# Performance work log

Measured on AMD Instinct MI355X. Metric: run time of the kernel, lower is better.

Reference implementation:

```python
import jax, jax.numpy as jnp
import numpy as np

DN = ('NCDHW', 'OIDHW', 'NCDHW')

def conv3d(x, w, b, stride=1, padding=1, lhs_dilation=1):
    pad = [(padding, padding)] * 3 if isinstance(padding, int) else padding
    y = jax.lax.conv_general_dilated(
        x, w, window_strides=(stride,) * 3, padding=pad,
        lhs_dilation=(lhs_dilation,) * 3, dimension_numbers=DN)
    return y + b[None, :, None, None, None]

def bool_to_multichannel(x):
    # (B,1,D,H,W) bool -> (B,8,D/4,H/4,W/4) float; each 4x4x4 patch bit-packed to 8 bytes
    B = x.shape[0]; D = x.shape[2]; d = D // 4
    p = x.reshape(B, d, 4, d, 4, d, 4)
    p = p.transpose(0, 1, 3, 5, 2, 4, 6).reshape(B, d, d, d, 8, 8)
    pw2 = (2.0 ** jnp.arange(8)).astype(jnp.float32)
    mc = jnp.sum(p.astype(jnp.float32) * pw2, axis=-1)  # (B,d,d,d,8)
    return mc.transpose(0, 4, 1, 2, 3) / 255.0

def setup_inputs():
    key = jax.random.key(0)
    ks = jax.random.split(key, 26)
    B, RES = 4, 256
    CH, E, ZC, K = 32, 16, 128, 8192
    L = 16  # latent resolution (mc res 64 / 2^(len(ch_mult)-1))
    # block-sparse boolean voxels so a good fraction of latent patches is all-zero
    coarse = jax.random.uniform(ks[0], (B, 1, 16, 16, 16)) < 0.6
    coarse = jnp.repeat(jnp.repeat(jnp.repeat(coarse, 16, 2), 16, 3), 16, 4)
    dense = jax.random.uniform(ks[1], (B, 1, RES, RES, RES)) < 0.3
    x = coarse & dense
    p = lambda k, shape, s=0.05: (jax.random.normal(k, shape) * s).astype(jnp.float32)
    return {
        'x': x,
        'enc_in_w': p(ks[2], (CH, 8, 3, 3, 3)), 'enc_in_b': p(ks[3], (CH,)),
        'enc_d1_w': p(ks[4], (2 * CH, CH, 3, 3, 3)), 'enc_d1_b': p(ks[5], (2 * CH,)),
        'enc_d2_w': p(ks[6], (4 * CH, 2 * CH, 3, 3, 3)), 'enc_d2_b': p(ks[7], (4 * CH,)),
        'enc_out_w': p(ks[8], (ZC, 4 * CH, 3, 3, 3)), 'enc_out_b': p(ks[9], (ZC,)),
        'quant_w': p(ks[10], (E, ZC, 1, 1, 1)), 'quant_b': p(ks[11], (E,)),
        'codebook': p(ks[12], (K, E), 0.5),
        'replacement_token': p(ks[13], (1, E), 0.02),
        'pos_embedding': p(ks[14], (1, E, L, L, L), 1.0),
        'post_quant_w': p(ks[15], (ZC, E, 1, 1, 1)), 'post_quant_b': p(ks[16], (ZC,)),
        'dec_in_w': p(ks[17], (ZC, ZC, 3, 3, 3)), 'dec_in_b': p(ks[18], (ZC,)),
        'dec_u1_w': p(ks[19], (2 * CH, ZC, 3, 3, 3)), 'dec_u1_b': p(ks[20], (2 * CH,)),
        'dec_u2_w': p(ks[21], (CH, 2 * CH, 3, 3, 3)), 'dec_u2_b': p(ks[22], (CH,)),
        'dec_out_w': p(ks[23], (8, CH, 3, 3, 3)), 'dec_out_b': p(ks[24], (8,)),
    }

def reference(x, enc_in_w, enc_in_b, enc_d1_w, enc_d1_b, enc_d2_w, enc_d2_b,
              enc_out_w, enc_out_b, quant_w, quant_b, codebook, replacement_token,
              pos_embedding, post_quant_w, post_quant_b, dec_in_w, dec_in_b,
              dec_u1_w, dec_u1_b, dec_u2_w, dec_u2_b, dec_out_w, dec_out_b):
    silu = jax.nn.silu
    mc = bool_to_multichannel(x)                      # (B,8,64,64,64)
    B, _, Dm, _, _ = mc.shape
    L = Dm // 4                                       # latent res = 16

    # zero-patch mask, patch_size=4 (== max_pool3d(nonzero_any) < 0.5)
    nz = jnp.any(mc != 0, axis=1)                     # (B,64,64,64)
    pooled = nz.reshape(B, L, 4, L, 4, L, 4).any(axis=(2, 4, 6))
    zero_mask = ~pooled.reshape(B, L * L * L)         # (B,N) True = all-zero patch

    # encoder (downsample x4) + quant_conv (1x1x1)
    h = silu(conv3d(mc, enc_in_w, enc_in_b))
    h = silu(conv3d(h, enc_d1_w, enc_d1_b, stride=2))
    h = silu(conv3d(h, enc_d2_w, enc_d2_b, stride=2))
    h = conv3d(h, enc_out_w, enc_out_b)
    h = conv3d(h, quant_w, quant_b, padding=0)        # (B,E,L,L,L)
    E = h.shape[1]
    seq = h.reshape(B, E, -1).transpose(0, 2, 1)      # (B,N,E)

    dist = jnp.sum(codebook * codebook, axis=-1) - 2.0 * jnp.einsum('bne,ke->bnk', seq, codebook)
    idx = jnp.argmin(dist, axis=-1)                   # (B,N)
    q_nz = codebook[idx]                              # (B,N,E)
    nonzero = ~zero_mask
    # commit over nonzero tokens * non_mask_frac == masked mean over all tokens
    mse_tok = jnp.mean(jnp.square(jax.lax.stop_gradient(q_nz) - seq), axis=-1)
    commit_loss = 0.25 * jnp.mean(jnp.where(nonzero, mse_tok, 0.0))

    # replacement token is index 0 of the full codebook; real codes shift by +1
    full_idx = jnp.where(zero_mask, 0, idx + 1)       # (B,N)
    full_cb = jnp.concatenate([replacement_token, codebook], axis=0)
    quant = full_cb[full_idx].transpose(0, 2, 1).reshape(B, E, L, L, L)

    # decoder (upsample x4 via fractionally-strided convs)
    q = quant + pos_embedding
    q = conv3d(q, post_quant_w, post_quant_b, padding=0)
    d = silu(conv3d(q, dec_in_w, dec_in_b))
    d = silu(conv3d(d, dec_u1_w, dec_u1_b, padding=[(2, 1)] * 3, lhs_dilation=2))
    d = silu(conv3d(d, dec_u2_w, dec_u2_b, padding=[(2, 1)] * 3, lhs_dilation=2))
    recon = conv3d(d, dec_out_w, dec_out_b)           # (B,8,64,64,64)
    return recon, mc, commit_loss, full_idx
```

## Files before the change

### kernel.cpp

```cpp
#include <hip/hip_runtime.h>
#include <hip/hip_bf16.h>
#include <math.h>

#define BB 4
#define NTOK 4096
#define KCB 8192
#define ED 16

__device__ __forceinline__ float silu_f(float x){ return x / (1.0f + expf(-x)); }
__device__ __forceinline__ double silu_d(double x){ return x / (1.0 + exp(-x)); }

template<typename T> struct V4T { typedef T type __attribute__((ext_vector_type(4))); };
typedef float f2v __attribute__((ext_vector_type(2)));

__global__ void r9_probe_zero(int* flags){ if (threadIdx.x < 2) flags[threadIdx.x] = 0; }

__global__ void r17_probe(const unsigned char* __restrict__ x, int* __restrict__ flags){
  __shared__ int so, sa;
  if (threadIdx.x == 0){ so = 0; sa = 0; }
  __syncthreads();
  const uint4* p = (const uint4*)x + (size_t)(blockIdx.x*256 + threadIdx.x)*4;
  unsigned uo = 0, ua = 0;
  #pragma unroll
  for (int r=0;r<4;++r){
    uint4 v = p[r];
    unsigned uw = v.x | v.y | v.z | v.w;
    uo |= (uw & 0xFFFFFF00u);
    ua |= (uw & 0x000000FFu);
  }
  if (uo) so = 1;
  if (ua) sa = 1;
  __syncthreads();
  if (threadIdx.x == 0){
    if (so) atomicOr(flags + 0, 1);
    if (sa) atomicOr(flags + 1, 1);
  }
}

__global__ void r9_pack_mc(const unsigned char* __restrict__ x, float* __restrict__ mc,
                           const int* __restrict__ flags){
  int t = blockIdx.x*256 + threadIdx.x;
  int k = t & 63, j = (t>>6)&63, i = (t>>12)&63, b = t>>18;
  int is_i32 = (flags[1] != 0) && (flags[0] == 0);
  unsigned ch[8];
  #pragma unroll
  for (int q=0;q<8;++q) ch[q]=0u;
  if (is_i32){
    const int* xb = (const int*)x + ((size_t)b << 24);
    #pragma unroll
    for (int a=0;a<4;++a){
      #pragma unroll
      for (int b2=0;b2<4;++b2){
        const int4 v = *(const int4*)(xb + (((size_t)(4*i+a))<<16) + ((size_t)(4*j+b2)<<8) + (size_t)(4*k));
        int vv[4] = {v.x, v.y, v.z, v.w};
        #pragma unroll
        for (int c2=0;c2<4;++c2){
          int lin = a*16 + b2*4 + c2;
          unsigned bit = vv[c2] ? 1u : 0u;
          ch[lin>>3] += bit << (lin&7);
        }
      }
    }
  } else {
    const unsigned char* xb = x + ((size_t)b << 24);
    #pragma unroll
    for (int a=0;a<4;++a){
      #pragma unroll
      for (int b2=0;b2<4;++b2){
        const unsigned char* row = xb + (((size_t)(4*i+a))<<16) + ((size_t)(4*j+b2)<<8) + (size_t)(4*k);
        unsigned v = *(const unsigned*)row;
        #pragma unroll
        for (int c2=0;c2<4;++c2){
          int lin = a*16 + b2*4 + c2;
          unsigned bit = ((v >> (8*c2)) & 0xffu) ? 1u : 0u;
          ch[lin>>3] += bit << (lin&7);
        }
      }
    }
  }
  size_t sp = ((size_t)i<<12) + (j<<6) + k;
  #pragma unroll
  for (int q=0;q<8;++q)
    mc[(((size_t)(b*8+q))<<18) + sp] = (float)ch[q] / 255.0f;
}

__global__ void r9_token_nz(const float* __restrict__ mc, unsigned char* __restrict__ tnz){
  int t = blockIdx.x*64 + threadIdx.x;
  int tk = t&15, tj=(t>>4)&15, ti=(t>>8)&15, b=t>>12;
  bool any = false;
  for (int q=0;q<8 && !any;++q){
    const float* mq = mc + (((size_t)(b*8+q))<<18);
    for (int a=0;a<4;++a)
      for (int c=0;c<4;++c){
        const float4 v = *(const float4*)(mq + ((size_t)(4*ti+a)<<12) + ((size_t)(4*tj+c)<<6) + (size_t)(4*tk));
        if (v.x!=0.f || v.y!=0.f || v.z!=0.f || v.w!=0.f){ any = true; }
      }
  }
  tnz[t] = any ? 1 : 0;
}

template<int XT, int STRIDE, typename TIN, typename ACC>
__device__ __forceinline__ void load_span(const TIN* __restrict__ inr, bool xlo, bool xhi,
                                          ACC (&xv)[STRIDE*(XT-1)+3]){
  static_assert(XT==4, "XT must be 4");
  typedef typename V4T<TIN>::type tin4;
  if (STRIDE==1){
    tin4 m = *(const tin4*)(inr + 1);
    xv[1]=(ACC)m.x; xv[2]=(ACC)m.y; xv[3]=(ACC)m.z; xv[4]=(ACC)m.w;
    xv[0] = xlo ? (ACC)inr[0] : (ACC)0;
    xv[5] = xhi ? (ACC)inr[5] : (ACC)0;
  } else {
    tin4 a = *(const tin4*)(inr + 1);
    tin4 b = *(const tin4*)(inr + 5);
    xv[1]=(ACC)a.x; xv[2]=(ACC)a.y; xv[3]=(ACC)a.z; xv[4]=(ACC)a.w;
    xv[5]=(ACC)b.x; xv[6]=(ACC)b.y; xv[7]=(ACC)b.z; xv[8]=(ACC)b.w;
    xv[0] = xlo ? (ACC)inr[0] : (ACC)0;
  }
}

template<int CIN, int OCB, int XT, int STRIDE, bool DOSILU, typename TIN, typename TOUT, typename ACC>
__global__ void r16_conv3x3(const TIN* __restrict__ in, const float* __restrict__ w,
                            const float* __restrict__ bias, TOUT* __restrict__ out,
                            int Din, int Dout){
  constexpr int SPAN = STRIDE*(XT-1)+3;
  const int oc0 = blockIdx.y * OCB;
  const int n3 = Dout*Dout*Dout;
  const int nxt = Dout / XT;
  const int t = blockIdx.x*256 + threadIdx.x;
  const int xo0 = (t % nxt)*XT;
  const int yo = (t/nxt)%Dout, zo = t/(nxt*Dout);
  const int zi0 = zo*STRIDE-1, yi0 = yo*STRIDE-1, xi0 = xo0*STRIDE-1;
  const bool xlo = (xi0 >= 0);
  const bool xhi = (xi0 + (SPAN-1) < Din);

  ACC acc[OCB][XT];
  #pragma unroll
  for (int q=0;q<OCB;++q){
    ACC bv = (ACC)bias[oc0+q];
    #pragma unroll
    for (int s=0;s<XT;++s) acc[q][s] = bv;
  }

  #pragma unroll 1
  for (int i=0;i<CIN;++i){
    const TIN* inc = in + (size_t)i*Din*Din*Din;
    const float* wci = w + ((size_t)oc0*CIN + i)*27;
    #pragma unroll
    for (int kd=0;kd<3;++kd){
      int z = zi0+kd; if ((unsigned)z >= (unsigned)Din) continue;
      #pragma unroll
      for (int kh=0;kh<3;++kh){
        int y = yi0+kh; if ((unsigned)y >= (unsigned)Din) continue;
        const TIN* inr = inc + ((size_t)z*Din + y)*Din + xi0;
        ACC xv[SPAN];
        load_span<XT,STRIDE,TIN,ACC>(inr, xlo, xhi, xv);
        #pragma unroll
        for (int q=0;q<OCB;++q){
          const float* wr = wci + (size_t)q*CIN*27 + kd*9 + kh*3;
          #pragma unroll
          for (int kw=0;kw<3;++kw){
            ACC wv = (ACC)wr[kw];
            #pragma unroll
            for (int s=0;s<XT;++s)
              acc[q][s] = fma(wv, xv[s*STRIDE+kw], acc[q][s]);
          }
        }
      }
    }
  }
  if (DOSILU){
    #pragma unroll
    for (int q=0;q<OCB;++q)
      #pragma unroll
      for (int s=0;s<XT;++s){
        if (sizeof(ACC)==8) acc[q][s] = (ACC)silu_d((double)acc[q][s]);
        else                acc[q][s] = (ACC)silu_f((float)acc[q][s]);
      }
  }
  size_t vox = ((size_t)zo*Dout + yo)*Dout + xo0;
  #pragma unroll
  for (int q=0;q<OCB;++q)
    #pragma unroll
    for (int s=0;s<XT;++s)
      out[(size_t)(oc0+q)*n3 + vox + s] = (TOUT)acc[q][s];
}

template<int CIN, int OCB, int XT, int NS, int STRIDE, typename TIN, typename ACC>
__global__ void r16_conv_part(const TIN* __restrict__ in, const float* __restrict__ w,
                              const float* __restrict__ bias, ACC* __restrict__ part,
                              int Din, int Dout){
  constexpr int SPAN = STRIDE*(XT-1)+3;
  const int oc0 = blockIdx.y * OCB;
  const int OC  = gridDim.y * OCB;
  const int cz  = blockIdx.z;
  const int n3 = Dout*Dout*Dout;
  const int nxt = Dout / XT;
  const int t = blockIdx.x*256 + threadIdx.x;
  const int xo0 = (t % nxt)*XT;
  const int yo = (t/nxt)%Dout, zo = t/(nxt*Dout);
  const int zi0 = zo*STRIDE-1, yi0 = yo*STRIDE-1, xi0 = xo0*STRIDE-1;
  const bool xlo = (xi0 >= 0);
  const bool xhi = (xi0 + (SPAN-1) < Din);

  ACC acc[OCB][XT];
  #pragma unroll
  for (int q=0;q<OCB;++q){
    ACC bv = (cz==0) ? (ACC)bias[oc0+q] : (ACC)0;
    #pragma unroll
    for (int s=0;s<XT;++s) acc[q][s] = bv;
  }

  const int cbeg = cz * (CIN/NS);
  #pragma unroll 1
  for (int i=cbeg; i<cbeg + CIN/NS; ++i){
    const TIN* inc = in + (size_t)i*Din*Din*Din;
    const float* wci = w + ((size_t)oc0*CIN + i)*27;
    #pragma unroll
    for (int kd=0;kd<3;++kd){
      int z = zi0+kd; if ((unsigned)z >= (unsigned)Din) continue;
      #pragma unroll
      for (int kh=0;kh<3;++kh){
        int y = yi0+kh; if ((unsigned)y >= (unsigned)Din) continue;
        const TIN* inr = inc + ((size_t)z*Din + y)*Din + xi0;
        ACC xv[SPAN];
        load_span<XT,STRIDE,TIN,ACC>(inr, xlo, xhi, xv);
        #pragma unroll
        for (int q=0;q<OCB;++q){
          const float* wr = wci + (size_t)q*CIN*27 + kd*9 + kh*3;
          #pragma unroll
          for (int kw=0;kw<3;++kw){
            ACC wv = (ACC)wr[kw];
            #pragma unroll
            for (int s=0;s<XT;++s)
              acc[q][s] = fma(wv, xv[s*STRIDE+kw], acc[q][s]);
          }
        }
      }
    }
  }
  size_t vox = ((size_t)zo*Dout + yo)*Dout + xo0;
  #pragma unroll
  for (int q=0;q<OCB;++q)
    #pragma unroll
    for (int s=0;s<XT;++s)
      part[((size_t)cz*OC + (oc0+q))*n3 + vox + s] = acc[q][s];
}

template<int CIN, int OCB, int XT, int NS, int STRIDE, typename TIN, typename ACC>
__global__ void r18_conv_part_b(const TIN* __restrict__ in_all, size_t in_bstride,
                                const float* __restrict__ w, const float* __restrict__ bias,
                                ACC* __restrict__ part, int Din, int Dout){
  constexpr int SPAN = STRIDE*(XT-1)+3;
  const int oc0 = blockIdx.y * OCB;
  const int OC  = gridDim.y * OCB;
  const int bz  = blockIdx.z / NS;
  const int cz  = blockIdx.z % NS;
  const TIN* in = in_all + (size_t)bz*in_bstride;
  const int n3 = Dout*Dout*Dout;
  const int nxt = Dout / XT;
  const int t = blockIdx.x*256 + threadIdx.x;
  const int xo0 = (t % nxt)*XT;
  const int yo = (t/nxt)%Dout, zo = t/(nxt*Dout);
  const int zi0 = zo*STRIDE-1, yi0 = yo*STRIDE-1, xi0 = xo0*STRIDE-1;
  const bool xlo = (xi0 >= 0);
  const bool xhi = (xi0 + (SPAN-1) < Din);

  ACC acc[OCB][XT];
  #pragma unroll
  for (int q=0;q<OCB;++q){
    ACC bv = (cz==0) ? (ACC)bias[oc0+q] : (ACC)0;
    #pragma unroll
    for (int s=0;s<XT;++s) acc[q][s] = bv;
  }

  const int cbeg = cz * (CIN/NS);
  #pragma unroll 1
  for (int i=cbeg; i<cbeg + CIN/NS; ++i){
    const TIN* inc = in + (size_t)i*Din*Din*Din;
    const float* wci = w + ((size_t)oc0*CIN + i)*27;
    #pragma unroll
    for (int kd=0;kd<3;++kd){
      int z = zi0+kd; if ((unsigned)z >= (unsigned)Din) continue;
      #pragma unroll
      for (int kh=0;kh<3;++kh){
        int y = yi0+kh; if ((unsigned)y >= (unsigned)Din) continue;
        const TIN* inr = inc + ((size_t)z*Din + y)*Din + xi0;
        ACC xv[SPAN];
        load_span<XT,STRIDE,TIN,ACC>(inr, xlo, xhi, xv);
        #pragma unroll
        for (int q=0;q<OCB;++q){
          const float* wr = wci + (size_t)q*CIN*27 + kd*9 + kh*3;
          #pragma unroll
          for (int kw=0;kw<3;++kw){
            ACC wv = (ACC)wr[kw];
            #pragma unroll
            for (int s=0;s<XT;++s)
              acc[q][s] = fma(wv, xv[s*STRIDE+kw], acc[q][s]);
          }
        }
      }
    }
  }
  size_t vox = ((size_t)zo*Dout + yo)*Dout + xo0;
  #pragma unroll
  for (int q=0;q<OCB;++q)
    #pragma unroll
    for (int s=0;s<XT;++s)
      part[((size_t)(bz*NS+cz)*OC + (oc0+q))*n3 + vox + s] = acc[q][s];
}

template<int NS, int VEC, bool DOSILU, typename ACC, typename TOUT>
__global__ void r16_reduce(const ACC* __restrict__ part, TOUT* __restrict__ out, int total){
  int t0 = (blockIdx.x*256 + threadIdx.x)*VEC;
  if (t0 >= total) return;
  ACC a[VEC];
  #pragma unroll
  for (int v=0;v<VEC;++v) a[v] = part[t0+v];
  #pragma unroll
  for (int s=1;s<NS;++s){
    #pragma unroll
    for (int v=0;v<VEC;++v) a[v] += part[(size_t)s*total + t0+v];
  }
  #pragma unroll
  for (int v=0;v<VEC;++v){
    if (DOSILU){
      if (sizeof(ACC)==8) a[v] = (ACC)silu_d((double)a[v]);
      else                a[v] = (ACC)silu_f((float)a[v]);
    }
    out[t0+v] = (TOUT)a[v];
  }
}

template<int NS, int VEC, bool DOSILU, typename ACC, typename TOUT>
__global__ void r18_reduce_b(const ACC* __restrict__ part, TOUT* __restrict__ out, int total){
  int b = blockIdx.y;
  int t0 = (blockIdx.x*256 + threadIdx.x)*VEC;
  if (t0 >= total) return;
  const ACC* pb = part + (size_t)b*NS*total;
  ACC a[VEC];
  #pragma unroll
  for (int v=0;v<VEC;++v) a[v] = pb[t0+v];
  #pragma unroll
  for (int s=1;s<NS;++s){
    #pragma unroll
    for (int v=0;v<VEC;++v) a[v] += pb[(size_t)s*total + t0+v];
  }
  #pragma unroll
  for (int v=0;v<VEC;++v){
    if (DOSILU){
      if (sizeof(ACC)==8) a[v] = (ACC)silu_d((double)a[v]);
      else                a[v] = (ACC)silu_f((float)a[v]);
    }
    out[(size_t)b*total + t0+v] = (TOUT)a[v];
  }
}

__global__ void r18_quantconv(const double* __restrict__ parts, const float* __restrict__ w,
                              const float* __restrict__ bias, double* __restrict__ seqd){
  int t = blockIdx.x*256 + threadIdx.x;
  int n = t & 4095, e = (t>>12)&15, b = t>>16;
  const double* p0 = parts + (size_t)(b*2+0)*524288 + n;
  const double* p1 = parts + (size_t)(b*2+1)*524288 + n;
  double acc = (double)bias[e];
  const float* we = w + e*128;
  for (int i=0;i<128;++i)
    acc = fma(p0[(size_t)i<<12] + p1[(size_t)i<<12], (double)we[i], acc);
  seqd[((size_t)(b*NTOK+n))*ED + e] = acc;
}

__global__ void r9_postquant_b(const float* __restrict__ qpeb, const float* __restrict__ w,
                               const float* __restrict__ bias, float* __restrict__ pqb){
  int t = blockIdx.x*256 + threadIdx.x;
  if (t >= 524288) return;
  int n = t & 4095, o = t >> 12;
  float acc = bias[o];
  const float* wo = w + o*16;
  #pragma unroll
  for (int e=0;e<16;++e) acc = fmaf(qpeb[((size_t)e<<12)+n], wo[e], acc);
  pqb[t] = acc;
}

__global__ void r9_cnorm(const float* __restrict__ cb, double* __restrict__ cnormd){
  int k = blockIdx.x*256 + threadIdx.x;
  if (k >= KCB) return;
  const float* c = cb + (size_t)k*ED;
  double s = 0.0;
  #pragma unroll
  for (int e=0;e<ED;++e) s = fma((double)c[e], (double)c[e], s);
  cnormd[k] = s;
}

#define VQC 256
#define VQPARTS 32
template<int PARTS>
__global__ void r18_vq_partial(const double* __restrict__ seqd, const float* __restrict__ cb,
                               const double* __restrict__ cnormd,
                               double* __restrict__ pdist, int* __restrict__ pidx){
  __shared__ double scb[VQC*ED];
  __shared__ double snorm[VQC];
  const int part = blockIdx.y;
  const int tok0 = blockIdx.x*256 + threadIdx.x;
  const int tok1 = tok0 + 8192;
  double s0[16], s1[16];
  const double* sr0 = seqd + (size_t)tok0*ED;
  const double* sr1 = seqd + (size_t)tok1*ED;
  #pragma unroll
  for (int e=0;e<16;++e){ s0[e] = sr0[e]; s1[e] = sr1[e]; }
  const int kbase = part * (KCB/PARTS);
  for (int u=threadIdx.x; u<VQC*ED; u+=256) scb[u] = (double)cb[(size_t)kbase*ED + u];
  for (int u=threadIdx.x; u<VQC; u+=256) snorm[u] = cnormd[kbase+u];
  __syncthreads();
  double best0 = 1.0e300, best1 = 1.0e300; int bi0 = 0, bi1 = 0;
  for (int kk=0; kk<VQC; ++kk){
    const double* cr = scb + kk*ED;
    double dot0 = 0.0, dot1 = 0.0;
    #pragma unroll
    for (int e=0;e<16;++e){
      double c = cr[e];
      dot0 = fma(s0[e], c, dot0);
      dot1 = fma(s1[e], c, dot1);
    }
    double nm = snorm[kk];
    double d0 = nm - 2.0*dot0;
    double d1 = nm - 2.0*dot1;
    if (d0 < best0){ best0 = d0; bi0 = kbase+kk; }
    if (d1 < best1){ best1 = d1; bi1 = kbase+kk; }
  }
  pdist[part*16384 + tok0] = best0;
  pidx [part*16384 + tok0] = bi0;
  pdist[part*16384 + tok1] = best1;
  pidx [part*16384 + tok1] = bi1;
}

template<int PARTS>
__global__ void r12_vq_merge(const double* __restrict__ pdist, const int* __restrict__ pidx,
                             const unsigned char* __restrict__ tnz, int* __restrict__ idxw,
                             float* __restrict__ out_idx, float* __restrict__ loss_slot){
  int tok = blockIdx.x*256 + threadIdx.x;
  if (tok == 0) *loss_slot = 0.f;
  double best = pdist[tok]; int bi = pidx[tok];
  #pragma unroll
  for (int p=1;p<PARTS;++p){
    double d2 = pdist[p*16384+tok];
    if (d2 < best){ best = d2; bi = pidx[p*16384+tok]; }
  }
  idxw[tok] = bi;
  out_idx[tok] = tnz[tok] ? (float)(bi+1) : 0.f;
}

__global__ void r9_commit(const double* __restrict__ seqd, const float* __restrict__ cb,
                          const int* __restrict__ idxw, const unsigned char* __restrict__ tnz,
                          float* __restrict__ loss_slot){
  int tok = blockIdx.x*256 + threadIdx.x;
  float v = 0.f;
  if (tnz[tok]){
    const float* c = cb + (size_t)idxw[tok]*ED;
    const double* s = seqd + (size_t)tok*ED;
    double acc = 0.0;
    #pragma unroll
    for (int e=0;e<ED;++e){ double d = (double)c[e]-s[e]; acc = fma(d,d,acc); }
    v = (float)(acc * (0.25/(16.0*16384.0)));
  }
  #pragma unroll
  for (int off=32; off; off>>=1) v += __shfl_down(v, off);
  if ((threadIdx.x & 63) == 0) atomicAdd(loss_slot, v);
}

__global__ void r9_gather_pos(const float* __restrict__ cb, const float* __restrict__ rep,
                              const int* __restrict__ idxw, const unsigned char* __restrict__ tnz,
                              const float* __restrict__ pos, float* __restrict__ qpe){
  int t = blockIdx.x*256 + threadIdx.x;
  int n = t & 4095, e = (t>>12)&15, b = t>>16;
  int tok = b*NTOK + n;
  float v = tnz[tok] ? cb[(size_t)idxw[tok]*ED + e] : rep[e];
  qpe[t] = v + pos[((size_t)e<<12) + n];
}

template<int CIN, int XT, bool DOSILU>
__global__ void r16_tconv(const float* __restrict__ in, const float* __restrict__ w,
                          const float* __restrict__ bias, float* __restrict__ out,
                          int Din){
  static_assert(XT==2, "XT must be 2");
  const int oc = blockIdx.y;
  const int nxt = Din / XT;
  const int t = blockIdx.x*256 + threadIdx.x;
  const int ux0 = (t % nxt)*XT;
  const int uy = (t/nxt)%Din, uz = t/(nxt*Din);
  const bool vx = ux0 > 0, vy = uy > 0, vz = uz > 0;
  const int DD = Din*Din, n3 = DD*Din;

  float b0 = bias[oc];
  float acc[8][XT];
  #pragma unroll
  for (int q=0;q<8;++q)
    #pragma unroll
    for (int s=0;s<XT;++s) acc[q][s] = b0;

  const float* p = in + ((size_t)uz*Din + uy)*Din + ux0;
  #pragma unroll 1
  for (int i=0;i<CIN;++i){
    float X[2][2][XT+1];
    #pragma unroll
    for (int za=0; za<2; ++za){
      #pragma unroll
      for (int ya=0; ya<2; ++ya){
        bool okzy = (za==1 || vz) && (ya==1 || vy);
        const float* pr = p + (za-1)*DD + (ya-1)*Din;
        if (okzy){
          f2v m = *(const f2v*)(pr);
          X[za][ya][1] = m.x; X[za][ya][2] = m.y;
          X[za][ya][0] = vx ? pr[-1] : 0.f;
        } else {
          X[za][ya][0] = 0.f; X[za][ya][1] = 0.f; X[za][ya][2] = 0.f;
        }
      }
    }
    const float* wi = w + ((size_t)(oc*CIN) + i)*27;
    #pragma unroll
    for (int kd=0;kd<3;++kd){
      #pragma unroll
      for (int kh=0;kh<3;++kh){
        #pragma unroll
        for (int kw=0;kw<3;++kw){
          const int pz = (kd==1) ? 1 : 0, py = (kh==1) ? 1 : 0, px = (kw==1) ? 1 : 0;
          const int za = (kd==0) ? 0 : 1, ya = (kh==0) ? 0 : 1, xa = (kw==0) ? 0 : 1;
          float wv = wi[kd*9+kh*3+kw];
          #pragma unroll
          for (int s=0;s<XT;++s)
            acc[pz*4+py*2+px][s] = fmaf(wv, X[za][ya][s+xa], acc[pz*4+py*2+px][s]);
        }
      }
    }
    p += n3;
  }
  if (DOSILU){
    #pragma unroll
    for (int q=0;q<8;++q)
      #pragma unroll
      for (int s=0;s<XT;++s) acc[q][s] = silu_f(acc[q][s]);
  }
  const int Dout = 2*Din;
  #pragma unroll
  for (int pz=0; pz<2; ++pz){
    #pragma unroll
    for (int py=0; py<2; ++py){
      float* row = out + (((size_t)oc*Dout + 2*uz+pz)*Dout + (2*uy+py))*Dout + 2*ux0;
      #pragma unroll
      for (int s=0;s<XT;++s){
        float2 v2 = make_float2(acc[pz*4+py*2+0][s], acc[pz*4+py*2+1][s]);
        *(float2*)(row + 2*s) = v2;
      }
    }
  }
}

template<int CIN, int XT, int NS>
__global__ void r16_tconv_part(const float* __restrict__ in, const float* __restrict__ w,
                               const float* __restrict__ bias, float* __restrict__ part,
                               int Din){
  static_assert(XT==2, "XT must be 2");
  const int oc = blockIdx.y;
  const int OC = gridDim.y;
  const int cz = blockIdx.z;
  const int nxt = Din / XT;
  const int t = blockIdx.x*256 + threadIdx.x;
  const int ux0 = (t % nxt)*XT;
  const int uy = (t/nxt)%Din, uz = t/(nxt*Din);
  const bool vx = ux0 > 0, vy = uy > 0, vz = uz > 0;
  const int DD = Din*Din, n3 = DD*Din;

  float b0 = (cz==0) ? bias[oc] : 0.f;
  float acc[8][XT];
  #pragma unroll
  for (int q=0;q<8;++q)
    #pragma unroll
    for (int s=0;s<XT;++s) acc[q][s] = b0;

  const int cbeg = cz * (CIN/NS);
  const float* p = in + (size_t)cbeg*n3 + ((size_t)uz*Din + uy)*Din + ux0;
  #pragma unroll 1
  for (int i=cbeg; i<cbeg + CIN/NS; ++i){
    float X[2][2][XT+1];
    #pragma unroll
    for (int za=0; za<2; ++za){
      #pragma unroll
      for (int ya=0; ya<2; ++ya){
        bool okzy = (za==1 || vz) && (ya==1 || vy);
        const float* pr = p + (za-1)*DD + (ya-1)*Din;
        if (okzy){
          f2v m = *(const f2v*)(pr);
          X[za][ya][1] = m.x; X[za][ya][2] = m.y;
          X[za][ya][0] = vx ? pr[-1] : 0.f;
        } else {
          X[za][ya][0] = 0.f; X[za][ya][1] = 0.f; X[za][ya][2] = 0.f;
        }
      }
    }
    const float* wi = w + ((size_t)(oc*CIN) + i)*27;
    #pragma unroll
    for (int kd=0;kd<3;++kd){
      #pragma unroll
      for (int kh=0;kh<3;++kh){
        #pragma unroll
        for (int kw=0;kw<3;++kw){
          const int pz = (kd==1) ? 1 : 0, py = (kh==1) ? 1 : 0, px = (kw==1) ? 1 : 0;
          const int za = (kd==0) ? 0 : 1, ya = (kh==0) ? 0 : 1, xa = (kw==0) ? 0 : 1;
          float wv = wi[kd*9+kh*3+kw];
          #pragma unroll
          for (int s=0;s<XT;++s)
            acc[pz*4+py*2+px][s] = fmaf(wv, X[za][ya][s+xa], acc[pz*4+py*2+px][s]);
        }
      }
    }
    p += n3;
  }
  const int Dout = 2*Din;
  const size_t n3out = (size_t)Dout*Dout*Dout;
  float* pb = part + (size_t)cz*OC*n3out;
  #pragma unroll
  for (int pz=0; pz<2; ++pz){
    #pragma unroll
    for (int py=0; py<2; ++py){
      float* row = pb + (((size_t)oc*Dout + 2*uz+pz)*Dout + (2*uy+py))*Dout + 2*ux0;
      #pragma unroll
      for (int s=0;s<XT;++s){
        float2 v2 = make_float2(acc[pz*4+py*2+0][s], acc[pz*4+py*2+1][s]);
        *(float2*)(row + 2*s) = v2;
      }
    }
  }
}

__global__ void r9_diag_ws(float* out0, float v){
  if (threadIdx.x == 0 && blockIdx.x == 0) out0[0] = v;
}

extern "C" void kernel_launch(void* const* d_in, const int* in_sizes, int n_in,
                              void* d_out, int out_size, void* d_ws, size_t ws_size,
                              hipStream_t stream){
  const unsigned char* x = (const unsigned char*)d_in[0];
  const float* enc_in_w  = (const float*)d_in[1];
  const float* enc_in_b  = (const float*)d_in[2];
  const float* enc_d1_w  = (const float*)d_in[3];
  const float* enc_d1_b  = (const float*)d_in[4];
  const float* enc_d2_w  = (const float*)d_in[5];
  const float* enc_d2_b  = (const float*)d_in[6];
  const float* enc_out_w = (const float*)d_in[7];
  const float* enc_out_b = (const float*)d_in[8];
  const float* quant_w   = (const float*)d_in[9];
  const float* quant_b   = (const float*)d_in[10];
  const float* codebook  = (const float*)d_in[11];
  const float* rep_tok   = (const float*)d_in[12];
  const float* pos_emb   = (const float*)d_in[13];
  const float* pq_w      = (const float*)d_in[14];
  const float* pq_b      = (const float*)d_in[15];
  const float* dec_in_w  = (const float*)d_in[16];
  const float* dec_in_b  = (const float*)d_in[17];
  const float* dec_u1_w  = (const float*)d_in[18];
  const float* dec_u1_b  = (const float*)d_in[19];
  const float* dec_u2_w  = (const float*)d_in[20];
  const float* dec_u2_b  = (const float*)d_in[21];
  const float* dec_out_w = (const float*)d_in[22];
  const float* dec_out_b = (const float*)d_in[23];

  float* out = (float*)d_out;
  const size_t OFF_RECON = 0;
  const size_t OFF_MC    = 8388608;
  const size_t OFF_LOSS  = 16777216;
  const size_t OFF_IDX   = 16777217;

  char* wsb = (char*)d_ws;
  float*  Sbig  = (float*) (wsb + 0);
  float*  Shd   = (float*) (wsb + 33554432);
  float*  Spq   = (float*) (wsb + 50331648);
  float*  SdD   = (float*) (wsb + 52428800);
  double* seqd  = (double*)(wsb + 54525952);
  double* cnormd= (double*)(wsb + 56623104);
  int*    idxw  = (int*)   (wsb + 57475072);
  unsigned char* tnz = (unsigned char*)(wsb + 57540608);
  float*  qpe   = (float*) (wsb + 57556992);
  int*    dflag = (int*)   (wsb + 58605568);
  const size_t WS_NEEDED = 58605632;

  double* scr_d  = (double*)wsb;
  float*  scr_f  = (float*)wsb;
  float*  scr_f2 = (float*)(wsb + 33554432);
  double* h3     = (double*)(wsb + 33554432);
  double* pdist  = (double*)wsb;
  int*    pidx   = (int*)(wsb + VQPARTS*16384*8);
  float* h2all = out + OFF_RECON;

  dim3 blk(256);

  if (ws_size < WS_NEEDED){
    r9_diag_ws<<<dim3(1), dim3(64), 0, stream>>>(out + OFF_RECON,
        9.0e6f + (float)(ws_size >> 20));
    return;
  }

  r9_probe_zero<<<dim3(1), dim3(64), 0, stream>>>(dflag);
  r17_probe<<<dim3(256), blk, 0, stream>>>(x, dflag);

  r9_pack_mc<<<dim3(4096), blk, 0, stream>>>(x, out + OFF_MC, dflag);
  r9_token_nz<<<dim3(256), dim3(64), 0, stream>>>(out + OFF_MC, tnz);

  for (int b = 0; b < BB; ++b){
    const float* mcb = out + OFF_MC + (size_t)b*8*262144;
    r16_conv3x3<8,8,4,1,true,float,float,double>  <<<dim3(256,4,1), blk, 0, stream>>>(mcb,  enc_in_w, enc_in_b, Sbig, 64, 64);
    r16_conv3x3<32,4,4,2,true,float,float,double> <<<dim3(32,16,1), blk, 0, stream>>>(Sbig, enc_d1_w, enc_d1_b, h2all + (size_t)b*2097152, 64, 32);
  }
  r18_conv_part_b<64,4,4,2,2,float,double><<<dim3(4,32,8), blk, 0, stream>>>(h2all, 2097152, enc_d2_w, enc_d2_b, scr_d, 32, 16);
  r18_reduce_b<2,2,true,double,double><<<dim3(1024,4), blk, 0, stream>>>(scr_d, h3, 524288);
  r18_conv_part_b<128,4,4,2,1,double,double><<<dim3(4,32,8), blk, 0, stream>>>(h3, 524288, enc_out_w, enc_out_b, scr_d, 16, 16);
  r18_quantconv<<<dim3(1024), blk, 0, stream>>>(scr_d, quant_w, quant_b, seqd);

  r9_cnorm<<<dim3(32), blk, 0, stream>>>(codebook, cnormd);
  r18_vq_partial<VQPARTS><<<dim3(32,VQPARTS), blk, 0, stream>>>(seqd, codebook, cnormd, pdist, pidx);
  r12_vq_merge<VQPARTS><<<dim3(64), blk, 0, stream>>>(pdist, pidx, tnz, idxw, out + OFF_IDX, out + OFF_LOSS);
  r9_commit<<<dim3(64), blk, 0, stream>>>(seqd, codebook, idxw, tnz, out + OFF_LOSS);

  r9_gather_pos<<<dim3(1024), blk, 0, stream>>>(codebook, rep_tok, idxw, tnz, pos_emb, qpe);
  for (int b = 0; b < BB; ++b){
    const float* qpeb = qpe + (size_t)b*65536;
    float* reconb = out + OFF_RECON + (size_t)b*8*262144;
    r9_postquant_b<<<dim3(2048), blk, 0, stream>>>(qpeb, pq_w, pq_b, Spq);
    r16_conv_part<128,4,4,8,1,float,float><<<dim3(4,32,8), blk, 0, stream>>>(Spq, dec_in_w, dec_in_b, scr_f, 16, 16);
    r16_reduce<8,4,true,float,float><<<dim3(512), blk, 0, stream>>>(scr_f, SdD, 524288);
    r16_tconv_part<128,2,2><<<dim3(8,64,2), blk, 0, stream>>>(SdD, dec_u1_w, dec_u1_b, scr_f2, 16);
    r16_reduce<2,4,true,float,float><<<dim3(2048), blk, 0, stream>>>(scr_f2, Shd, 2097152);
    r16_tconv<64,2,true> <<<dim3(64,32,1), blk, 0, stream>>>(Shd,  dec_u2_w, dec_u2_b, Sbig, 32);
    r16_conv_part<32,8,4,2,1,float,float><<<dim3(256,1,2), blk, 0, stream>>>(Sbig, dec_out_w, dec_out_b, scr_f2, 64, 64);
    r16_reduce<2,4,false,float,float><<<dim3(2048), blk, 0, stream>>>(scr_f2, reconb, 2097152);
  }
}
```

Baseline: 3.676 ms.

## Batch decoder front stages across all samples and drop tconv channel split

Decoder post-quant, dec_in conv and first transposed conv now run once over all four batch samples instead of per-sample loops, raising grid size and cutting launches. The first tconv no longer splits input channels into partials followed by a reduce; it accumulates all 128 channels and applies SiLU in place, writing into the recon output buffer as scratch. The encoder's second half is regrouped into two passes of two samples, with the d2 conv split into four partials per block. This trades fewer launches and reduce passes for longer per-thread loops and different workspace aliasing.

```diff
diff --git a/kernel.cpp b/kernel.cpp
--- a/kernel.cpp
+++ b/kernel.cpp
@@ -355,29 +355,34 @@
   }
 }
 
-__global__ void r18_quantconv(const double* __restrict__ parts, const float* __restrict__ w,
-                              const float* __restrict__ bias, double* __restrict__ seqd){
+__global__ void r19_quantconv4(const double* __restrict__ parts, const float* __restrict__ w,
+                               const float* __restrict__ bias, double* __restrict__ seqd, int bbase){
   int t = blockIdx.x*256 + threadIdx.x;
-  int n = t & 4095, e = (t>>12)&15, b = t>>16;
-  const double* p0 = parts + (size_t)(b*2+0)*524288 + n;
-  const double* p1 = parts + (size_t)(b*2+1)*524288 + n;
+  int n = t & 4095, e = (t>>12)&15, bp = t>>16;
+  const double* p0 = parts + (size_t)(bp*4+0)*524288 + n;
+  const double* p1 = parts + (size_t)(bp*4+1)*524288 + n;
+  const double* p2 = parts + (size_t)(bp*4+2)*524288 + n;
+  const double* p3 = parts + (size_t)(bp*4+3)*524288 + n;
   double acc = (double)bias[e];
   const float* we = w + e*128;
-  for (int i=0;i<128;++i)
-    acc = fma(p0[(size_t)i<<12] + p1[(size_t)i<<12], (double)we[i], acc);
-  seqd[((size_t)(b*NTOK+n))*ED + e] = acc;
-}
-
-__global__ void r9_postquant_b(const float* __restrict__ qpeb, const float* __restrict__ w,
-                               const float* __restrict__ bias, float* __restrict__ pqb){
+  for (int i=0;i<128;++i){
+    size_t o = (size_t)i<<12;
+    double val = ((p0[o]+p1[o])+p2[o])+p3[o];
+    acc = fma(val, (double)we[i], acc);
+  }
+  seqd[((size_t)((bbase+bp)*NTOK+n))*ED + e] = acc;
+}
+
+__global__ void r19_postquant_all(const float* __restrict__ qpe, const float* __restrict__ w,
+                                  const float* __restrict__ bias, float* __restrict__ pq_all){
   int t = blockIdx.x*256 + threadIdx.x;
-  if (t >= 524288) return;
-  int n = t & 4095, o = t >> 12;
+  int n = t & 4095, o = (t>>12)&127, b = t>>19;
+  const float* qpeb = qpe + (size_t)b*65536;
   float acc = bias[o];
   const float* wo = w + o*16;
   #pragma unroll
   for (int e=0;e<16;++e) acc = fmaf(qpeb[((size_t)e<<12)+n], wo[e], acc);
-  pqb[t] = acc;
+  pq_all[t] = acc;
 }
 
 __global__ void r9_cnorm(const float* __restrict__ cb, double* __restrict__ cnormd){
@@ -554,14 +559,15 @@
   }
 }
 
-template<int CIN, int XT, int NS>
-__global__ void r16_tconv_part(const float* __restrict__ in, const float* __restrict__ w,
-                               const float* __restrict__ bias, float* __restrict__ part,
-                               int Din){
+template<int CIN, int XT, bool DOSILU>
+__global__ void r19_tconv_b(const float* __restrict__ in_all, size_t in_bstride,
+                            const float* __restrict__ w, const float* __restrict__ bias,
+                            float* __restrict__ out_all, size_t out_bstride, int Din){
   static_assert(XT==2, "XT must be 2");
   const int oc = blockIdx.y;
-  const int OC = gridDim.y;
-  const int cz = blockIdx.z;
+  const int bz = blockIdx.z;
+  const float* in = in_all + (size_t)bz*in_bstride;
+  float* out = out_all + (size_t)bz*out_bstride;
   const int nxt = Din / XT;
   const int t = blockIdx.x*256 + threadIdx.x;
   const int ux0 = (t % nxt)*XT;
@@ -569,17 +575,16 @@
   const bool vx = ux0 > 0, vy = uy > 0, vz = uz > 0;
   const int DD = Din*Din, n3 = DD*Din;
 
-  float b0 = (cz==0) ? bias[oc] : 0.f;
+  float b0 = bias[oc];
   float acc[8][XT];
   #pragma unroll
   for (int q=0;q<8;++q)
     #pragma unroll
     for (int s=0;s<XT;++s) acc[q][s] = b0;
 
-  const int cbeg = cz * (CIN/NS);
-  const float* p = in + (size_t)cbeg*n3 + ((size_t)uz*Din + uy)*Din + ux0;
+  const float* p = in + ((size_t)uz*Din + uy)*Din + ux0;
   #pragma unroll 1
-  for (int i=cbeg; i<cbeg + CIN/NS; ++i){
+  for (int i=0;i<CIN;++i){
     float X[2][2][XT+1];
     #pragma unroll
     for (int za=0; za<2; ++za){
@@ -614,14 +619,18 @@
     }
     p += n3;
   }
+  if (DOSILU){
+    #pragma unroll
+    for (int q=0;q<8;++q)
+      #pragma unroll
+      for (int s=0;s<XT;++s) acc[q][s] = silu_f(acc[q][s]);
+  }
   const int Dout = 2*Din;
-  const size_t n3out = (size_t)Dout*Dout*Dout;
-  float* pb = part + (size_t)cz*OC*n3out;
   #pragma unroll
   for (int pz=0; pz<2; ++pz){
     #pragma unroll
     for (int py=0; py<2; ++py){
-      float* row = pb + (((size_t)oc*Dout + 2*uz+pz)*Dout + (2*uy+py))*Dout + 2*ux0;
+      float* row = out + (((size_t)oc*Dout + 2*uz+pz)*Dout + (2*uy+py))*Dout + 2*ux0;
       #pragma unroll
       for (int s=0;s<XT;++s){
         float2 v2 = make_float2(acc[pz*4+py*2+0][s], acc[pz*4+py*2+1][s]);
@@ -671,9 +680,6 @@
 
   char* wsb = (char*)d_ws;
   float*  Sbig  = (float*) (wsb + 0);
-  float*  Shd   = (float*) (wsb + 33554432);
-  float*  Spq   = (float*) (wsb + 50331648);
-  float*  SdD   = (float*) (wsb + 52428800);
   double* seqd  = (double*)(wsb + 54525952);
   double* cnormd= (double*)(wsb + 56623104);
   int*    idxw  = (int*)   (wsb + 57475072);
@@ -684,11 +690,14 @@
 
   double* scr_d  = (double*)wsb;
   float*  scr_f  = (float*)wsb;
+  float*  h2w    = (float*)(wsb + 33554432);
+  double* h3w    = (double*)(wsb + 33554432);
+  float*  pq_all = (float*)(wsb + 33554432);
+  float*  dD_all = (float*)(wsb + 41943040);
   float*  scr_f2 = (float*)(wsb + 33554432);
-  double* h3     = (double*)(wsb + 33554432);
   double* pdist  = (double*)wsb;
   int*    pidx   = (int*)(wsb + VQPARTS*16384*8);
-  float* h2all = out + OFF_RECON;
+  float*  u1_all = out + OFF_RECON;
 
   dim3 blk(256);
 
@@ -704,15 +713,18 @@
   r9_pack_mc<<<dim3(4096), blk, 0, stream>>>(x, out + OFF_MC, dflag);
   r9_token_nz<<<dim3(256), dim3(64), 0, stream>>>(out + OFF_MC, tnz);
 
-  for (int b = 0; b < BB; ++b){
-    const float* mcb = out + OFF_MC + (size_t)b*8*262144;
-    r16_conv3x3<8,8,4,1,true,float,float,double>  <<<dim3(256,4,1), blk, 0, stream>>>(mcb,  enc_in_w, enc_in_b, Sbig, 64, 64);
-    r16_conv3x3<32,4,4,2,true,float,float,double> <<<dim3(32,16,1), blk, 0, stream>>>(Sbig, enc_d1_w, enc_d1_b, h2all + (size_t)b*2097152, 64, 32);
-  }
-  r18_conv_part_b<64,4,4,2,2,float,double><<<dim3(4,32,8), blk, 0, stream>>>(h2all, 2097152, enc_d2_w, enc_d2_b, scr_d, 32, 16);
-  r18_reduce_b<2,2,true,double,double><<<dim3(1024,4), blk, 0, stream>>>(scr_d, h3, 524288);
-  r18_conv_part_b<128,4,4,2,1,double,double><<<dim3(4,32,8), blk, 0, stream>>>(h3, 524288, enc_out_w, enc_out_b, scr_d, 16, 16);
-  r18_quantconv<<<dim3(1024), blk, 0, stream>>>(scr_d, quant_w, quant_b, seqd);
+  for (int p = 0; p < 2; ++p){
+    for (int bp = 0; bp < 2; ++bp){
+      int b = 2*p + bp;
+      const float* mcb = out + OFF_MC + (size_t)b*8*262144;
+      r16_conv3x3<8,8,4,1,true,float,float,double>  <<<dim3(256,4,1), blk, 0, stream>>>(mcb,  enc_in_w, enc_in_b, Sbig, 64, 64);
+      r16_conv3x3<32,4,4,2,true,float,float,double> <<<dim3(32,16,1), blk, 0, stream>>>(Sbig, enc_d1_w, enc_d1_b, h2w + (size_t)bp*2097152, 64, 32);
+    }
+    r18_conv_part_b<64,4,4,4,2,float,double><<<dim3(4,32,8), blk, 0, stream>>>(h2w, 2097152, enc_d2_w, enc_d2_b, scr_d, 32, 16);
+    r18_reduce_b<4,2,true,double,double><<<dim3(1024,2), blk, 0, stream>>>(scr_d, h3w, 524288);
+    r18_conv_part_b<128,4,4,4,1,double,double><<<dim3(4,32,8), blk, 0, stream>>>(h3w, 524288, enc_out_w, enc_out_b, scr_d, 16, 16);
+    r19_quantconv4<<<dim3(512), blk, 0, stream>>>(scr_d, quant_w, quant_b, seqd, 2*p);
+  }
 
   r9_cnorm<<<dim3(32), blk, 0, stream>>>(codebook, cnormd);
   r18_vq_partial<VQPARTS><<<dim3(32,VQPARTS), blk, 0, stream>>>(seqd, codebook, cnormd, pdist, pidx);
@@ -720,15 +732,13 @@
   r9_commit<<<dim3(64), blk, 0, stream>>>(seqd, codebook, idxw, tnz, out + OFF_LOSS);
 
   r9_gather_pos<<<dim3(1024), blk, 0, stream>>>(codebook, rep_tok, idxw, tnz, pos_emb, qpe);
+  r19_postquant_all<<<dim3(8192), blk, 0, stream>>>(qpe, pq_w, pq_b, pq_all);
+  r18_conv_part_b<128,4,4,4,1,float,float><<<dim3(4,32,16), blk, 0, stream>>>(pq_all, 524288, dec_in_w, dec_in_b, scr_f, 16, 16);
+  r18_reduce_b<4,4,true,float,float><<<dim3(512,4), blk, 0, stream>>>(scr_f, dD_all, 524288);
+  r19_tconv_b<128,2,true><<<dim3(8,64,4), blk, 0, stream>>>(dD_all, 524288, dec_u1_w, dec_u1_b, u1_all, 2097152, 16);
   for (int b = 0; b < BB; ++b){
-    const float* qpeb = qpe + (size_t)b*65536;
-    float* reconb = out + OFF_RECON + (size_t)b*8*262144;
-    r9_postquant_b<<<dim3(2048), blk, 0, stream>>>(qpeb, pq_w, pq_b, Spq);
-    r16_conv_part<128,4,4,8,1,float,float><<<dim3(4,32,8), blk, 0, stream>>>(Spq, dec_in_w, dec_in_b, scr_f, 16, 16);
-    r16_reduce<8,4,true,float,float><<<dim3(512), blk, 0, stream>>>(scr_f, SdD, 524288);
-    r16_tconv_part<128,2,2><<<dim3(8,64,2), blk, 0, stream>>>(SdD, dec_u1_w, dec_u1_b, scr_f2, 16);
-    r16_reduce<2,4,true,float,float><<<dim3(2048), blk, 0, stream>>>(scr_f2, Shd, 2097152);
-    r16_tconv<64,2,true> <<<dim3(64,32,1), blk, 0, stream>>>(Shd,  dec_u2_w, dec_u2_b, Sbig, 32);
+    float* reconb = out + OFF_RECON + (size_t)b*2097152;
+    r16_tconv<64,2,true> <<<dim3(64,32,1), blk, 0, stream>>>(u1_all + (size_t)b*2097152, dec_u2_w, dec_u2_b, Sbig, 32);
     r16_conv_part<32,8,4,2,1,float,float><<<dim3(256,1,2), blk, 0, stream>>>(Sbig, dec_out_w, dec_out_b, scr_f2, 64, 64);
     r16_reduce<2,4,false,float,float><<<dim3(2048), blk, 0, stream>>>(scr_f2, reconb, 2097152);
   }
```

Result: faster. 3.579 ms (-2.6%).
